# Kernel tuning notes

Measured on AMD Instinct MI355X. Metric: run time of the kernel, lower is better.

The kernel has to match this reference:

```python
import jax, jax.numpy as jnp
import numpy as np

B, N, DEG = 128, 512, 8          # graphs, nodes per graph, avg degree
E = B * N * DEG                  # 524288 edges
F_IN, H1, H2, C = 128, 64, 128, 10
RATIO = 0.8
K = int(np.ceil(RATIO * N))      # TopKPooling keeps ceil(0.8*N)=410 nodes per graph


def setup_inputs() -> dict:
    key = jax.random.key(0)
    ks = jax.random.split(key, 10)
    n_nodes = B * N
    x = jax.random.normal(ks[0], (n_nodes, F_IN), dtype=jnp.float32)
    # random intra-graph edges, then offset node ids per graph
    src = jax.random.randint(ks[1], (B, N * DEG), 0, N)
    dst = jax.random.randint(ks[2], (B, N * DEG), 0, N)
    off = (jnp.arange(B) * N)[:, None]
    edge_index = jnp.stack([(src + off).reshape(-1), (dst + off).reshape(-1)]).astype(jnp.int64)
    batch = jnp.repeat(jnp.arange(B), N).astype(jnp.int64)
    s1 = 1.0 / np.sqrt(F_IN)
    s2 = 1.0 / np.sqrt(H1)
    s3 = 1.0 / np.sqrt(H2)
    return {
        "x": x,
        "edge_index": edge_index,
        "batch": batch,
        "W1": jax.random.uniform(ks[3], (F_IN, H1), jnp.float32, -s1, s1),
        "b1": jnp.zeros((H1,), jnp.float32),
        "W2": jax.random.uniform(ks[4], (H1, H2), jnp.float32, -s2, s2),
        "b2": jnp.zeros((H2,), jnp.float32),
        "pool_w": jax.random.uniform(ks[5], (H2,), jnp.float32, -s3, s3),
        "fc_W": jax.random.uniform(ks[6], (H2, C), jnp.float32, -s3, s3),
        "fc_b": jax.random.uniform(ks[7], (C,), jnp.float32, -s3, s3),
    }


def gcn_conv(x, W, b, src, dst, num_nodes):
    # PyG GCNConv: add self-loops, symmetric normalization, scatter-add aggregation
    loop = jnp.arange(num_nodes)
    src = jnp.concatenate([src, loop])
    dst = jnp.concatenate([dst, loop])
    deg = jax.ops.segment_sum(jnp.ones_like(src, dtype=x.dtype), dst, num_segments=num_nodes)
    dis = jnp.where(deg > 0, jax.lax.rsqrt(jnp.maximum(deg, 1.0)), 0.0)
    norm = dis[src] * dis[dst]                       # [E+N]
    h = x @ W                                        # transform first (smaller of the two in conv1)
    out = jax.ops.segment_sum(norm[:, None] * h[src], dst, num_segments=num_nodes)
    return out + b


def reference(x, edge_index, batch, W1, b1, W2, b2, pool_w, fc_W, fc_b):
    num_nodes = x.shape[0]
    src, dst = edge_index[0], edge_index[1]
    x = jax.nn.relu(gcn_conv(x, W1, b1, src, dst, num_nodes))
    x = jax.nn.relu(gcn_conv(x, W2, b2, src, dst, num_nodes))
    # TopKPooling: score = (x . w)/||w||, per-graph top-k on raw score, gate by tanh(score)
    score = (x @ pool_w) / jnp.linalg.norm(pool_w)   # [B*N]
    score_b = score.reshape(B, N)
    top_vals, top_idx = jax.lax.top_k(score_b, K)    # [B, K]
    x_b = x.reshape(B, N, H2)
    x_sel = jnp.take_along_axis(x_b, top_idx[:, :, None], axis=1)   # [B, K, H2]
    x_sel = x_sel * jnp.tanh(top_vals)[:, :, None]
    # global max pool over each (pooled) graph; pooled edge_index is unused downstream
    g = jnp.max(x_sel, axis=1)                        # [B, H2]
    logits = g @ fc_W + fc_b                          # [B, C]
    return jax.nn.log_softmax(logits, axis=1)
```

## Files before the change

### kernel.cpp

```cpp
#include <hip/hip_runtime.h>
#include <hip/hip_bf16.h>


#define BB 128
#define NN 512
#define NODES (BB*NN)
#define EE (BB*NN*8)
#define EDGPG (NN*8)
#define F_IN 128
#define H1 64
#define H2 128
#define NC 10
#define KSEL 410
#define ROWCAP 48

typedef unsigned short u16;
typedef unsigned int   u32;

static __device__ __forceinline__ float lo2f(u32 u){ return __uint_as_float(u << 16); }
static __device__ __forceinline__ float hi2f(u32 u){ return __uint_as_float(u & 0xffff0000u); }
static __device__ __forceinline__ u16 f2b(float f){
    __hip_bfloat16 h = __float2bfloat16(f);
    return *reinterpret_cast<u16*>(&h);
}
static __device__ __forceinline__ u32 packbf(float a, float b){
    return (u32)f2b(a) | ((u32)f2b(b) << 16);
}
static __device__ __forceinline__ void acc8s(float* a, uint4 v, float ds){
    a[0] = fmaf(ds, lo2f(v.x), a[0]); a[1] = fmaf(ds, hi2f(v.x), a[1]);
    a[2] = fmaf(ds, lo2f(v.y), a[2]); a[3] = fmaf(ds, hi2f(v.y), a[3]);
    a[4] = fmaf(ds, lo2f(v.z), a[4]); a[5] = fmaf(ds, hi2f(v.z), a[5]);
    a[6] = fmaf(ds, lo2f(v.w), a[6]); a[7] = fmaf(ds, hi2f(v.w), a[7]);
}
static __device__ __forceinline__ void acc8(float* a, uint4 v){
    a[0] += lo2f(v.x); a[1] += hi2f(v.x);
    a[2] += lo2f(v.y); a[3] += hi2f(v.y);
    a[4] += lo2f(v.z); a[5] += hi2f(v.z);
    a[6] += lo2f(v.w); a[7] += hi2f(v.w);
}
static __device__ __forceinline__ int swz2048(int bid){
    return ((bid & 7) << 8) | (bid >> 3);
}

static __device__ __forceinline__ bool ei_is_i64(const int* __restrict__ ei){
    return ((ei[1] | ei[3] | ei[5] | ei[7]) == 0);
}
static __device__ __forceinline__ int ld_src(const int* __restrict__ ei, int e, bool w64){
    return w64 ? ei[2*e] : ei[e];
}
static __device__ __forceinline__ int ld_dst(const int* __restrict__ ei, int e, bool w64){
    return w64 ? ei[2*(EE + e)] : ei[EE + e];
}

#define G1NODES 64
#define XPAD 68
__global__ __launch_bounds__(512) void k_prep_gemm1(const int* __restrict__ ei,
                                                    const float* __restrict__ x,
                                                    const float* __restrict__ W1,
                                                    int* __restrict__ cnt,
                                                    int* __restrict__ adj,
                                                    u32* __restrict__ h1u){
    __shared__ __align__(16) float Ws[64*H1];
    __shared__ __align__(16) float xs[G1NODES*XPAD];
    bool w64 = ei_is_i64(ei);
    int t = threadIdx.x;
    int gb = (int)blockIdx.x;
    int b  = gb >> 3;
    int sub = gb & 7;
    int node0 = b*NN + sub*G1NODES;

    int e = b*EDGPG + sub*512 + t;
    int dv = (ld_dst(ei, e, w64) - b*NN) & (NN - 1);
    int sv = ld_src(ei, e, w64) & (NODES - 1);
    int anode = b*NN + dv;
    int p = ROWCAP;

    int tc = t & 15, tr = t >> 4;
    int j0 = tc*4, n0 = tr*2;
    float acc[2][4] = {};

    {
        const float4* Wv0 = (const float4*)W1;
        for (int i = t; i < 1024; i += 512)
            *(float4*)&Ws[i*4] = Wv0[i];
        for (int i = t; i < 1024; i += 512){
            int node = i >> 4, c = i & 15;
            *(float4*)&xs[node*XPAD + c*4] =
                *(const float4*)(x + (size_t)(node0 + node)*F_IN + c*4);
        }
    }
    __syncthreads();
    p = atomicAdd(&cnt[anode], 1);
    const float4* Wv1 = (const float4*)(W1 + 4096);
    float4 wr0 = Wv1[t], wr1 = Wv1[t + 512];
    float4 xr0 = *(const float4*)(x + (size_t)(node0 + (t >> 4))*F_IN + 64 + (t & 15)*4);
    float4 xr1 = *(const float4*)(x + (size_t)(node0 + ((t+512) >> 4))*F_IN + 64 + ((t+512) & 15)*4);

    #pragma unroll 2
    for (int k = 0; k < 64; k += 4){
        float4 xv0 = *(const float4*)&xs[(n0+0)*XPAD + k];
        float4 xv1 = *(const float4*)&xs[(n0+1)*XPAD + k];
        float xa0[4] = {xv0.x, xv0.y, xv0.z, xv0.w};
        float xa1[4] = {xv1.x, xv1.y, xv1.z, xv1.w};
        #pragma unroll
        for (int kk = 0; kk < 4; ++kk){
            float4 wv = *(const float4*)&Ws[(k+kk)*H1 + j0];
            acc[0][0] += xa0[kk]*wv.x; acc[0][1] += xa0[kk]*wv.y; acc[0][2] += xa0[kk]*wv.z; acc[0][3] += xa0[kk]*wv.w;
            acc[1][0] += xa1[kk]*wv.x; acc[1][1] += xa1[kk]*wv.y; acc[1][2] += xa1[kk]*wv.z; acc[1][3] += xa1[kk]*wv.w;
        }
    }
    __syncthreads();
    *(float4*)&Ws[(t      )*4] = wr0;
    *(float4*)&Ws[(t + 512)*4] = wr1;
    *(float4*)&xs[((t      ) >> 4)*XPAD + ((t      ) & 15)*4] = xr0;
    *(float4*)&xs[((t + 512) >> 4)*XPAD + ((t + 512) & 15)*4] = xr1;
    __syncthreads();
    #pragma unroll 2
    for (int k = 0; k < 64; k += 4){
        float4 xv0 = *(const float4*)&xs[(n0+0)*XPAD + k];
        float4 xv1 = *(const float4*)&xs[(n0+1)*XPAD + k];
        float xa0[4] = {xv0.x, xv0.y, xv0.z, xv0.w};
        float xa1[4] = {xv1.x, xv1.y, xv1.z, xv1.w};
        #pragma unroll
        for (int kk = 0; kk < 4; ++kk){
            float4 wv = *(const float4*)&Ws[(k+kk)*H1 + j0];
            acc[0][0] += xa0[kk]*wv.x; acc[0][1] += xa0[kk]*wv.y; acc[0][2] += xa0[kk]*wv.z; acc[0][3] += xa0[kk]*wv.w;
            acc[1][0] += xa1[kk]*wv.x; acc[1][1] += xa1[kk]*wv.y; acc[1][2] += xa1[kk]*wv.z; acc[1][3] += xa1[kk]*wv.w;
        }
    }
    if (p < ROWCAP - 1) adj[anode*ROWCAP + 1 + p] = sv;
    if (t < G1NODES){
        int node = node0 + t;
        adj[node*ROWCAP] = node;
    }
    #pragma unroll
    for (int i = 0; i < 2; ++i){
        int node = node0 + n0 + i;
        size_t base = (size_t)node*32 + tc*2;
        h1u[base]     = packbf(acc[i][0], acc[i][1]);
        h1u[base + 1] = packbf(acc[i][2], acc[i][3]);
    }
}

__global__ __launch_bounds__(256) void k_agg1(const uint4* __restrict__ h1v,
                                              const int* __restrict__ cnt,
                                              const int* __restrict__ adj,
                                              const float4* __restrict__ b1v,
                                              uint4* __restrict__ a1v){
    __shared__ float disl[NN];
    int t = threadIdx.x;
    int lb = swz2048((int)blockIdx.x);
    int node0 = lb*32;
    int node = node0 + (t >> 3);
    int fl = t & 7;
    int rs = node*ROWCAP;
    int cp = cnt[node];
    int4 ap0 = *(const int4*)&adj[rs];
    int4 ap1 = *(const int4*)&adj[rs + 4];
    uint4 vself = h1v[(size_t)node*8 + fl];
    int gbase = node0 & ~(NN - 1);
    for (int i = t; i < NN; i += 256){
        int c = cnt[gbase + i]; if (c > ROWCAP-1) c = ROWCAP-1;
        disl[i] = rsqrtf((float)(c + 1));
    }
    __syncthreads();
    int c = cp; if (c > ROWCAP-1) c = ROWCAP-1;
    int pe = rs + c + 1;
    float a0[8] = {}, a1r[8] = {}, a2r[8] = {}, a3r[8] = {};
    int p = rs;
    if (p + 4 <= pe){
        int s1 = ap0.y, s2 = ap0.z, s3 = ap0.w;
        float d0 = disl[node & (NN-1)];
        float d1 = disl[s1 & (NN-1)], d2 = disl[s2 & (NN-1)], d3 = disl[s3 & (NN-1)];
        uint4 v1 = h1v[s1*8 + fl];
        uint4 v2 = h1v[s2*8 + fl];
        uint4 v3 = h1v[s3*8 + fl];
        acc8s(a0, vself, d0); acc8s(a1r, v1, d1); acc8s(a2r, v2, d2); acc8s(a3r, v3, d3);
        p += 4;
    }
    if (p + 4 <= pe){
        int s0 = ap1.x, s1 = ap1.y, s2 = ap1.z, s3 = ap1.w;
        float d0 = disl[s0 & (NN-1)], d1 = disl[s1 & (NN-1)];
        float d2 = disl[s2 & (NN-1)], d3 = disl[s3 & (NN-1)];
        uint4 v0 = h1v[s0*8 + fl];
        uint4 v1 = h1v[s1*8 + fl];
        uint4 v2 = h1v[s2*8 + fl];
        uint4 v3 = h1v[s3*8 + fl];
        acc8s(a0, v0, d0); acc8s(a1r, v1, d1); acc8s(a2r, v2, d2); acc8s(a3r, v3, d3);
        p += 4;
    }
    for (; p + 4 <= pe; p += 4){
        int s0 = adj[p], s1 = adj[p+1], s2 = adj[p+2], s3 = adj[p+3];
        float d0 = disl[s0 & (NN-1)], d1 = disl[s1 & (NN-1)];
        float d2 = disl[s2 & (NN-1)], d3 = disl[s3 & (NN-1)];
        uint4 v0 = h1v[s0*8 + fl];
        uint4 v1 = h1v[s1*8 + fl];
        uint4 v2 = h1v[s2*8 + fl];
        uint4 v3 = h1v[s3*8 + fl];
        acc8s(a0, v0, d0); acc8s(a1r, v1, d1); acc8s(a2r, v2, d2); acc8s(a3r, v3, d3);
    }
    for (; p < pe; ++p){
        int s = adj[p];
        acc8s(a0, h1v[s*8 + fl], disl[s & (NN-1)]);
    }
    float r[8];
    #pragma unroll
    for (int j = 0; j < 8; ++j) r[j] = (a0[j] + a1r[j]) + (a2r[j] + a3r[j]);
    float dn = disl[node & (NN-1)];
    float4 bA = b1v[2*fl], bB = b1v[2*fl+1];
    float w0 = dn*r[0] + bA.x; w0 = w0 > 0.f ? w0 : 0.f;
    float w1 = dn*r[1] + bA.y; w1 = w1 > 0.f ? w1 : 0.f;
    float w2 = dn*r[2] + bA.z; w2 = w2 > 0.f ? w2 : 0.f;
    float w3 = dn*r[3] + bA.w; w3 = w3 > 0.f ? w3 : 0.f;
    float w4 = dn*r[4] + bB.x; w4 = w4 > 0.f ? w4 : 0.f;
    float w5 = dn*r[5] + bB.y; w5 = w5 > 0.f ? w5 : 0.f;
    float w6 = dn*r[6] + bB.z; w6 = w6 > 0.f ? w6 : 0.f;
    float w7 = dn*r[7] + bB.w; w7 = w7 > 0.f ? w7 : 0.f;
    a1v[node*8 + fl] = make_uint4(packbf(dn*w0, dn*w1), packbf(dn*w2, dn*w3),
                                  packbf(dn*w4, dn*w5), packbf(dn*w6, dn*w7));
}

#define G2NODES 32
#define APAD 68
__global__ __launch_bounds__(256) void k_gemm2s(const uint4* __restrict__ a1v,
                                                const int* __restrict__ cnt,
                                                const int* __restrict__ adj,
                                                const float* __restrict__ W2,
                                                const float* __restrict__ b2,
                                                const float* __restrict__ pw,
                                                u32* __restrict__ a2u,
                                                float* __restrict__ score){
    __shared__ __align__(16) float Ws[32*H2];
    __shared__ __align__(16) float as[G2NODES*APAD];
    __shared__ float pws[H2];
    int t = threadIdx.x;
    int lb = swz2048((int)blockIdx.x);
    int node0 = lb*G2NODES;
    int fl = t & 7, nl = t >> 3;
    int nodeg = node0 + nl;
    int rsg = nodeg*ROWCAP;
    int cp = cnt[nodeg];
    int4 ap0 = *(const int4*)&adj[rsg];
    int4 ap1 = *(const int4*)&adj[rsg + 4];
    uint4 vself = a1v[(size_t)nodeg*8 + fl];
    const float4* Wv0 = (const float4*)W2;
    float4 w0a = Wv0[t], w0b = Wv0[t+256], w0c = Wv0[t+512], w0d = Wv0[t+768];
    if (t < H2) pws[t] = pw[t];
    {
        int c = cp; if (c > ROWCAP-1) c = ROWCAP-1;
        int pe = rsg + c + 1;
        float a0[8] = {}, a1r[8] = {}, a2r[8] = {}, a3r[8] = {};
        int p = rsg;
        if (p + 4 <= pe){
            int s1 = ap0.y, s2 = ap0.z, s3 = ap0.w;
            uint4 v1 = a1v[s1*8 + fl];
            uint4 v2 = a1v[s2*8 + fl];
            uint4 v3 = a1v[s3*8 + fl];
            acc8(a0, vself); acc8(a1r, v1); acc8(a2r, v2); acc8(a3r, v3);
            p += 4;
        }
        if (p + 4 <= pe){
            int s0 = ap1.x, s1 = ap1.y, s2 = ap1.z, s3 = ap1.w;
            uint4 v0 = a1v[s0*8 + fl];
            uint4 v1 = a1v[s1*8 + fl];
            uint4 v2 = a1v[s2*8 + fl];
            uint4 v3 = a1v[s3*8 + fl];
            acc8(a0, v0); acc8(a1r, v1); acc8(a2r, v2); acc8(a3r, v3);
            p += 4;
        }
        for (; p + 4 <= pe; p += 4){
            int s0 = adj[p], s1 = adj[p+1], s2 = adj[p+2], s3 = adj[p+3];
            uint4 v0 = a1v[s0*8 + fl];
            uint4 v1 = a1v[s1*8 + fl];
            uint4 v2 = a1v[s2*8 + fl];
            uint4 v3 = a1v[s3*8 + fl];
            acc8(a0, v0); acc8(a1r, v1); acc8(a2r, v2); acc8(a3r, v3);
        }
        for (; p < pe; ++p){
            uint4 v = a1v[adj[p]*8 + fl];
            acc8(a0, v);
        }
        float dn = rsqrtf((float)(c + 1));
        float* dst = &as[nl*APAD + 8*fl];
        float r0 = dn*((a0[0] + a1r[0]) + (a2r[0] + a3r[0]));
        float r1 = dn*((a0[1] + a1r[1]) + (a2r[1] + a3r[1]));
        float r2 = dn*((a0[2] + a1r[2]) + (a2r[2] + a3r[2]));
        float r3 = dn*((a0[3] + a1r[3]) + (a2r[3] + a3r[3]));
        float r4 = dn*((a0[4] + a1r[4]) + (a2r[4] + a3r[4]));
        float r5 = dn*((a0[5] + a1r[5]) + (a2r[5] + a3r[5]));
        float r6 = dn*((a0[6] + a1r[6]) + (a2r[6] + a3r[6]));
        float r7 = dn*((a0[7] + a1r[7]) + (a2r[7] + a3r[7]));
        *(float4*)&dst[0] = make_float4(r0, r1, r2, r3);
        *(float4*)&dst[4] = make_float4(r4, r5, r6, r7);
    }
    *(float4*)&Ws[(t      )*4] = w0a;
    *(float4*)&Ws[(t + 256)*4] = w0b;
    *(float4*)&Ws[(t + 512)*4] = w0c;
    *(float4*)&Ws[(t + 768)*4] = w0d;
    __syncthreads();
    const float4* Wv1 = (const float4*)(W2 + 4096);
    float4 w1a = Wv1[t], w1b = Wv1[t+256], w1c = Wv1[t+512], w1d = Wv1[t+768];

    int tc = t & 31, tr = t >> 5;
    int j0 = tc*4, n0 = tr*4;
    float acc[4][4] = {};
    #pragma unroll
    for (int half = 0; half < 2; ++half){
        int kb = half*32;
        #pragma unroll 2
        for (int k = 0; k < 32; k += 4){
            float4 xv0 = *(const float4*)&as[(n0+0)*APAD + kb + k];
            float4 xv1 = *(const float4*)&as[(n0+1)*APAD + kb + k];
            float4 xv2 = *(const float4*)&as[(n0+2)*APAD + kb + k];
            float4 xv3 = *(const float4*)&as[(n0+3)*APAD + kb + k];
            float xa0[4] = {xv0.x, xv0.y, xv0.z, xv0.w};
            float xa1[4] = {xv1.x, xv1.y, xv1.z, xv1.w};
            float xa2[4] = {xv2.x, xv2.y, xv2.z, xv2.w};
            float xa3[4] = {xv3.x, xv3.y, xv3.z, xv3.w};
            #pragma unroll
            for (int kk = 0; kk < 4; ++kk){
                float4 wv = *(const float4*)&Ws[(k+kk)*H2 + j0];
                acc[0][0] += xa0[kk]*wv.x; acc[0][1] += xa0[kk]*wv.y; acc[0][2] += xa0[kk]*wv.z; acc[0][3] += xa0[kk]*wv.w;
                acc[1][0] += xa1[kk]*wv.x; acc[1][1] += xa1[kk]*wv.y; acc[1][2] += xa1[kk]*wv.z; acc[1][3] += xa1[kk]*wv.w;
                acc[2][0] += xa2[kk]*wv.x; acc[2][1] += xa2[kk]*wv.y; acc[2][2] += xa2[kk]*wv.z; acc[2][3] += xa2[kk]*wv.w;
                acc[3][0] += xa3[kk]*wv.x; acc[3][1] += xa3[kk]*wv.y; acc[3][2] += xa3[kk]*wv.z; acc[3][3] += xa3[kk]*wv.w;
            }
        }
        if (half == 0){
            __syncthreads();
            *(float4*)&Ws[(t      )*4] = w1a;
            *(float4*)&Ws[(t + 256)*4] = w1b;
            *(float4*)&Ws[(t + 512)*4] = w1c;
            *(float4*)&Ws[(t + 768)*4] = w1d;
            __syncthreads();
        }
    }
    float p0 = pws[j0], p1 = pws[j0+1], p2 = pws[j0+2], p3 = pws[j0+3];
    float bj0 = b2[j0], bj1 = b2[j0+1], bj2 = b2[j0+2], bj3 = b2[j0+3];
    #pragma unroll
    for (int i = 0; i < 4; ++i){
        float v0 = acc[i][0] + bj0; v0 = v0 > 0.f ? v0 : 0.f;
        float v1 = acc[i][1] + bj1; v1 = v1 > 0.f ? v1 : 0.f;
        float v2 = acc[i][2] + bj2; v2 = v2 > 0.f ? v2 : 0.f;
        float v3 = acc[i][3] + bj3; v3 = v3 > 0.f ? v3 : 0.f;
        size_t base = (size_t)(node0 + n0 + i)*64 + tc*2;
        a2u[base]     = packbf(v0, v1);
        a2u[base + 1] = packbf(v2, v3);
        float sp = v0*p0 + v1*p1 + v2*p2 + v3*p3;
        sp += __shfl_xor(sp, 16, 32);
        sp += __shfl_xor(sp,  8, 32);
        sp += __shfl_xor(sp,  4, 32);
        sp += __shfl_xor(sp,  2, 32);
        sp += __shfl_xor(sp,  1, 32);
        if (tc == 0) score[node0 + n0 + i] = sp;
    }
}

__global__ __launch_bounds__(512) void k_pool(const u32* __restrict__ a2u,
                                              const float* __restrict__ score,
                                              const float* __restrict__ pw,
                                              const float* __restrict__ fcW,
                                              const float* __restrict__ fcb,
                                              float* __restrict__ out){
    __shared__ float so[NN];
    __shared__ float ss[NN];
    __shared__ float th[NN];
    __shared__ float pm[32*H2];
    __shared__ float gl[H2];
    __shared__ float fws[H2*NC];
    __shared__ float lg[NC];
    __shared__ float red[3];
    int bid = blockIdx.x, t = threadIdx.x;
    int b = ((bid & 7) << 4) | (bid >> 3);
    float sc = score[b*NN + t];
    for (int i = t; i < H2*NC; i += 512) fws[i] = fcW[i];
    if (t < H2){ float v2 = pw[t]; gl[t] = v2*v2; }
    __syncthreads();
    if (t == 0){
        float s = 0.f;
        for (int i = 0; i < H2; ++i) s += gl[i];
        red[2] = rsqrtf(s);
    }
    __syncthreads();
    float pwinv = red[2];
    so[t] = sc; th[t] = tanhf(sc*pwinv);
    float v = sc;
    for (int k = 2; k <= NN; k <<= 1){
        for (int j = k >> 1; j > 0; j >>= 1){
            bool desc  = ((t & k) == 0);
            bool lower = ((t & j) == 0);
            bool wantmax = (desc == lower);
            float c;
            if (j >= 64){
                ss[t] = v; __syncthreads();
                c = ss[t ^ j];
                __syncthreads();
            } else {
                c = __shfl_xor(v, j, 64);
            }
            v = wantmax ? fmaxf(v, c) : fminf(v, c);
        }
    }
    ss[t] = v;
    __syncthreads();
    float thresh = ss[KSEL-1];
    float mask_t = (so[t] >= thresh) ? 0.f : -INFINITY;
    __syncthreads();
    so[t] = mask_t;
    __syncthreads();
    int tc = t & 15, q = t >> 4;
    const uint4* ap = (const uint4*)(a2u + (size_t)b*NN*64);
    float m0 = -INFINITY, m1 = -INFINITY, m2 = -INFINITY, m3 = -INFINITY;
    float m4 = -INFINITY, m5 = -INFINITY, m6 = -INFINITY, m7 = -INFINITY;
    int nb = q*16;
    #pragma unroll 4
    for (int n = nb; n < nb + 16; ++n){
        uint4 vv = ap[(size_t)n*16 + tc];
        float thn = th[n], son = so[n];
        m0 = fmaxf(m0, lo2f(vv.x)*thn + son);
        m1 = fmaxf(m1, hi2f(vv.x)*thn + son);
        m2 = fmaxf(m2, lo2f(vv.y)*thn + son);
        m3 = fmaxf(m3, hi2f(vv.y)*thn + son);
        m4 = fmaxf(m4, lo2f(vv.z)*thn + son);
        m5 = fmaxf(m5, hi2f(vv.z)*thn + son);
        m6 = fmaxf(m6, lo2f(vv.w)*thn + son);
        m7 = fmaxf(m7, hi2f(vv.w)*thn + son);
    }
    float* pmr = &pm[q*H2 + 8*tc];
    pmr[0] = m0; pmr[1] = m1; pmr[2] = m2; pmr[3] = m3;
    pmr[4] = m4; pmr[5] = m5; pmr[6] = m6; pmr[7] = m7;
    __syncthreads();
    if (t < H2){
        float g = pm[t];
        #pragma unroll
        for (int qq = 1; qq < 32; ++qq) g = fmaxf(g, pm[qq*H2 + t]);
        gl[t] = g;
    }
    __syncthreads();
    if (t < NC){
        float acc = fcb[t];
        for (int k2 = 0; k2 < H2; ++k2) acc += gl[k2]*fws[k2*NC + t];
        lg[t] = acc;
    }
    __syncthreads();
    if (t == 0){
        float mx = lg[0];
        for (int i = 1; i < NC; ++i) mx = fmaxf(mx, lg[i]);
        float s = 0.f;
        for (int i = 0; i < NC; ++i) s += expf(lg[i] - mx);
        red[0] = mx; red[1] = logf(s);
    }
    __syncthreads();
    if (t < NC) out[b*NC + t] = lg[t] - red[0] - red[1];
}

extern "C" void kernel_launch(void* const* d_in, const int* in_sizes, int n_in,
                              void* d_out, int out_size, void* d_ws, size_t ws_size,
                              hipStream_t stream) {
    const float* x   = (const float*)d_in[0];
    const int*   ei  = (const int*)d_in[1];
    const float* W1  = (const float*)d_in[3];
    const float* b1  = (const float*)d_in[4];
    const float* W2  = (const float*)d_in[5];
    const float* b2  = (const float*)d_in[6];
    const float* pw  = (const float*)d_in[7];
    const float* fcW = (const float*)d_in[8];
    const float* fcb = (const float*)d_in[9];

    char* ws = (char*)d_ws;
    int*   cnt   = (int*)(ws + 4096);
    float* score = (float*)(ws + 524288);
    int*   adj   = (int*)(ws + 4194304);
    u32*   h1u   = (u32*)(ws + 16777216);
    u32*   a1u   = (u32*)(ws + 25165824);
    u32*   a2u   = (u32*)(ws + 33554432);

    hipMemsetAsync(cnt, 0, NODES*sizeof(int), stream);
    k_prep_gemm1<<<NODES/G1NODES, 512, 0, stream>>>(ei, x, W1, cnt, adj, h1u);
    k_agg1<<<NODES/32, 256, 0, stream>>>((const uint4*)h1u, cnt, adj,
                                         (const float4*)b1, (uint4*)a1u);
    k_gemm2s<<<NODES/G2NODES, 256, 0, stream>>>((const uint4*)a1u, cnt, adj,
                                                W2, b2, pw, a2u, score);
    k_pool<<<BB, 512, 0, stream>>>(a2u, score, pw, fcW, fcb, (float*)d_out);
}
```

Baseline: 163.3 us.

## Store adjacency as 16-bit local indices and unroll first 16 neighbors

```diff
diff --git a/kernel.cpp b/kernel.cpp
--- a/kernel.cpp
+++ b/kernel.cpp
@@ -41,6 +41,9 @@
 static __device__ __forceinline__ int swz2048(int bid){
     return ((bid & 7) << 8) | (bid >> 3);
 }
+static __device__ __forceinline__ int swz1024(int bid){
+    return ((bid & 7) << 7) | (bid >> 3);
+}
 
 static __device__ __forceinline__ bool ei_is_i64(const int* __restrict__ ei){
     return ((ei[1] | ei[3] | ei[5] | ei[7]) == 0);
@@ -58,20 +61,20 @@
                                                     const float* __restrict__ x,
                                                     const float* __restrict__ W1,
                                                     int* __restrict__ cnt,
-                                                    int* __restrict__ adj,
+                                                    u16* __restrict__ adj,
                                                     u32* __restrict__ h1u){
     __shared__ __align__(16) float Ws[64*H1];
     __shared__ __align__(16) float xs[G1NODES*XPAD];
     bool w64 = ei_is_i64(ei);
     int t = threadIdx.x;
-    int gb = (int)blockIdx.x;
+    int gb = swz1024((int)blockIdx.x);
     int b  = gb >> 3;
     int sub = gb & 7;
     int node0 = b*NN + sub*G1NODES;
 
     int e = b*EDGPG + sub*512 + t;
     int dv = (ld_dst(ei, e, w64) - b*NN) & (NN - 1);
-    int sv = ld_src(ei, e, w64) & (NODES - 1);
+    int sv = ld_src(ei, e, w64) & (NN - 1);
     int anode = b*NN + dv;
     int p = ROWCAP;
 
@@ -128,10 +131,10 @@
             acc[1][0] += xa1[kk]*wv.x; acc[1][1] += xa1[kk]*wv.y; acc[1][2] += xa1[kk]*wv.z; acc[1][3] += xa1[kk]*wv.w;
         }
     }
-    if (p < ROWCAP - 1) adj[anode*ROWCAP + 1 + p] = sv;
+    if (p < ROWCAP - 1) adj[(size_t)anode*ROWCAP + 1 + p] = (u16)sv;
     if (t < G1NODES){
         int node = node0 + t;
-        adj[node*ROWCAP] = node;
+        adj[(size_t)node*ROWCAP] = (u16)(node & (NN - 1));
     }
     #pragma unroll
     for (int i = 0; i < 2; ++i){
@@ -144,69 +147,91 @@
 
 __global__ __launch_bounds__(256) void k_agg1(const uint4* __restrict__ h1v,
                                               const int* __restrict__ cnt,
-                                              const int* __restrict__ adj,
+                                              const u16* __restrict__ adj,
                                               const float4* __restrict__ b1v,
                                               uint4* __restrict__ a1v){
     __shared__ float disl[NN];
     int t = threadIdx.x;
     int lb = swz2048((int)blockIdx.x);
     int node0 = lb*32;
+    int gbase = node0 & ~(NN - 1);
     int node = node0 + (t >> 3);
+    int nl = node & (NN - 1);
     int fl = t & 7;
-    int rs = node*ROWCAP;
+    size_t rs = (size_t)node*ROWCAP;
     int cp = cnt[node];
-    int4 ap0 = *(const int4*)&adj[rs];
-    int4 ap1 = *(const int4*)&adj[rs + 4];
+    uint4 apA = *(const uint4*)&adj[rs];
+    uint4 apB = *(const uint4*)&adj[rs + 8];
     uint4 vself = h1v[(size_t)node*8 + fl];
-    int gbase = node0 & ~(NN - 1);
     for (int i = t; i < NN; i += 256){
         int c = cnt[gbase + i]; if (c > ROWCAP-1) c = ROWCAP-1;
         disl[i] = rsqrtf((float)(c + 1));
     }
     __syncthreads();
     int c = cp; if (c > ROWCAP-1) c = ROWCAP-1;
-    int pe = rs + c + 1;
+    int ne = c + 1;
+    int e1 = (int)(apA.x >> 16);
+    int e2 = (int)(apA.y & 0xffff), e3 = (int)(apA.y >> 16);
+    int e4 = (int)(apA.z & 0xffff), e5 = (int)(apA.z >> 16);
+    int e6 = (int)(apA.w & 0xffff), e7 = (int)(apA.w >> 16);
+    int e8  = (int)(apB.x & 0xffff), e9  = (int)(apB.x >> 16);
+    int e10 = (int)(apB.y & 0xffff), e11 = (int)(apB.y >> 16);
+    int e12 = (int)(apB.z & 0xffff), e13 = (int)(apB.z >> 16);
+    int e14 = (int)(apB.w & 0xffff), e15 = (int)(apB.w >> 16);
     float a0[8] = {}, a1r[8] = {}, a2r[8] = {}, a3r[8] = {};
-    int p = rs;
-    if (p + 4 <= pe){
-        int s1 = ap0.y, s2 = ap0.z, s3 = ap0.w;
-        float d0 = disl[node & (NN-1)];
-        float d1 = disl[s1 & (NN-1)], d2 = disl[s2 & (NN-1)], d3 = disl[s3 & (NN-1)];
-        uint4 v1 = h1v[s1*8 + fl];
-        uint4 v2 = h1v[s2*8 + fl];
-        uint4 v3 = h1v[s3*8 + fl];
+    int p = 0;
+    if (p + 4 <= ne){
+        float d0 = disl[nl], d1 = disl[e1], d2 = disl[e2], d3 = disl[e3];
+        uint4 v1 = h1v[(size_t)(gbase + e1)*8 + fl];
+        uint4 v2 = h1v[(size_t)(gbase + e2)*8 + fl];
+        uint4 v3 = h1v[(size_t)(gbase + e3)*8 + fl];
         acc8s(a0, vself, d0); acc8s(a1r, v1, d1); acc8s(a2r, v2, d2); acc8s(a3r, v3, d3);
         p += 4;
     }
-    if (p + 4 <= pe){
-        int s0 = ap1.x, s1 = ap1.y, s2 = ap1.z, s3 = ap1.w;
-        float d0 = disl[s0 & (NN-1)], d1 = disl[s1 & (NN-1)];
-        float d2 = disl[s2 & (NN-1)], d3 = disl[s3 & (NN-1)];
-        uint4 v0 = h1v[s0*8 + fl];
-        uint4 v1 = h1v[s1*8 + fl];
-        uint4 v2 = h1v[s2*8 + fl];
-        uint4 v3 = h1v[s3*8 + fl];
+    if (p + 4 <= ne){
+        float d0 = disl[e4], d1 = disl[e5], d2 = disl[e6], d3 = disl[e7];
+        uint4 v0 = h1v[(size_t)(gbase + e4)*8 + fl];
+        uint4 v1 = h1v[(size_t)(gbase + e5)*8 + fl];
+        uint4 v2 = h1v[(size_t)(gbase + e6)*8 + fl];
+        uint4 v3 = h1v[(size_t)(gbase + e7)*8 + fl];
         acc8s(a0, v0, d0); acc8s(a1r, v1, d1); acc8s(a2r, v2, d2); acc8s(a3r, v3, d3);
         p += 4;
     }
-    for (; p + 4 <= pe; p += 4){
-        int s0 = adj[p], s1 = adj[p+1], s2 = adj[p+2], s3 = adj[p+3];
-        float d0 = disl[s0 & (NN-1)], d1 = disl[s1 & (NN-1)];
-        float d2 = disl[s2 & (NN-1)], d3 = disl[s3 & (NN-1)];
-        uint4 v0 = h1v[s0*8 + fl];
-        uint4 v1 = h1v[s1*8 + fl];
-        uint4 v2 = h1v[s2*8 + fl];
-        uint4 v3 = h1v[s3*8 + fl];
+    if (p + 4 <= ne){
+        float d0 = disl[e8], d1 = disl[e9], d2 = disl[e10], d3 = disl[e11];
+        uint4 v0 = h1v[(size_t)(gbase + e8 )*8 + fl];
+        uint4 v1 = h1v[(size_t)(gbase + e9 )*8 + fl];
+        uint4 v2 = h1v[(size_t)(gbase + e10)*8 + fl];
+        uint4 v3 = h1v[(size_t)(gbase + e11)*8 + fl];
         acc8s(a0, v0, d0); acc8s(a1r, v1, d1); acc8s(a2r, v2, d2); acc8s(a3r, v3, d3);
-    }
-    for (; p < pe; ++p){
-        int s = adj[p];
-        acc8s(a0, h1v[s*8 + fl], disl[s & (NN-1)]);
+        p += 4;
+    }
+    if (p + 4 <= ne){
+        float d0 = disl[e12], d1 = disl[e13], d2 = disl[e14], d3 = disl[e15];
+        uint4 v0 = h1v[(size_t)(gbase + e12)*8 + fl];
+        uint4 v1 = h1v[(size_t)(gbase + e13)*8 + fl];
+        uint4 v2 = h1v[(size_t)(gbase + e14)*8 + fl];
+        uint4 v3 = h1v[(size_t)(gbase + e15)*8 + fl];
+        acc8s(a0, v0, d0); acc8s(a1r, v1, d1); acc8s(a2r, v2, d2); acc8s(a3r, v3, d3);
+        p += 4;
+    }
+    for (; p + 4 <= ne; p += 4){
+        int s0 = adj[rs+p], s1 = adj[rs+p+1], s2 = adj[rs+p+2], s3 = adj[rs+p+3];
+        float d0 = disl[s0], d1 = disl[s1], d2 = disl[s2], d3 = disl[s3];
+        uint4 v0 = h1v[(size_t)(gbase + s0)*8 + fl];
+        uint4 v1 = h1v[(size_t)(gbase + s1)*8 + fl];
+        uint4 v2 = h1v[(size_t)(gbase + s2)*8 + fl];
+        uint4 v3 = h1v[(size_t)(gbase + s3)*8 + fl];
+        acc8s(a0, v0, d0); acc8s(a1r, v1, d1); acc8s(a2r, v2, d2); acc8s(a3r, v3, d3);
+    }
+    for (; p < ne; ++p){
+        int s = adj[rs + p];
+        acc8s(a0, h1v[(size_t)(gbase + s)*8 + fl], disl[s]);
     }
     float r[8];
     #pragma unroll
     for (int j = 0; j < 8; ++j) r[j] = (a0[j] + a1r[j]) + (a2r[j] + a3r[j]);
-    float dn = disl[node & (NN-1)];
+    float dn = disl[nl];
     float4 bA = b1v[2*fl], bB = b1v[2*fl+1];
     float w0 = dn*r[0] + bA.x; w0 = w0 > 0.f ? w0 : 0.f;
     float w1 = dn*r[1] + bA.y; w1 = w1 > 0.f ? w1 : 0.f;
@@ -224,7 +249,7 @@
 #define APAD 68
 __global__ __launch_bounds__(256) void k_gemm2s(const uint4* __restrict__ a1v,
                                                 const int* __restrict__ cnt,
-                                                const int* __restrict__ adj,
+                                                const u16* __restrict__ adj,
                                                 const float* __restrict__ W2,
                                                 const float* __restrict__ b2,
                                                 const float* __restrict__ pw,
@@ -236,49 +261,72 @@
     int t = threadIdx.x;
     int lb = swz2048((int)blockIdx.x);
     int node0 = lb*G2NODES;
+    int gbase = node0 & ~(NN - 1);
     int fl = t & 7, nl = t >> 3;
     int nodeg = node0 + nl;
-    int rsg = nodeg*ROWCAP;
+    size_t rsg = (size_t)nodeg*ROWCAP;
     int cp = cnt[nodeg];
-    int4 ap0 = *(const int4*)&adj[rsg];
-    int4 ap1 = *(const int4*)&adj[rsg + 4];
+    uint4 apA = *(const uint4*)&adj[rsg];
+    uint4 apB = *(const uint4*)&adj[rsg + 8];
     uint4 vself = a1v[(size_t)nodeg*8 + fl];
     const float4* Wv0 = (const float4*)W2;
     float4 w0a = Wv0[t], w0b = Wv0[t+256], w0c = Wv0[t+512], w0d = Wv0[t+768];
     if (t < H2) pws[t] = pw[t];
     {
         int c = cp; if (c > ROWCAP-1) c = ROWCAP-1;
-        int pe = rsg + c + 1;
+        int ne = c + 1;
+        int e1 = (int)(apA.x >> 16);
+        int e2 = (int)(apA.y & 0xffff), e3 = (int)(apA.y >> 16);
+        int e4 = (int)(apA.z & 0xffff), e5 = (int)(apA.z >> 16);
+        int e6 = (int)(apA.w & 0xffff), e7 = (int)(apA.w >> 16);
+        int e8  = (int)(apB.x & 0xffff), e9  = (int)(apB.x >> 16);
+        int e10 = (int)(apB.y & 0xffff), e11 = (int)(apB.y >> 16);
+        int e12 = (int)(apB.z & 0xffff), e13 = (int)(apB.z >> 16);
+        int e14 = (int)(apB.w & 0xffff), e15 = (int)(apB.w >> 16);
         float a0[8] = {}, a1r[8] = {}, a2r[8] = {}, a3r[8] = {};
-        int p = rsg;
-        if (p + 4 <= pe){
-            int s1 = ap0.y, s2 = ap0.z, s3 = ap0.w;
-            uint4 v1 = a1v[s1*8 + fl];
-            uint4 v2 = a1v[s2*8 + fl];
-            uint4 v3 = a1v[s3*8 + fl];
+        int p = 0;
+        if (p + 4 <= ne){
+            uint4 v1 = a1v[(size_t)(gbase + e1)*8 + fl];
+            uint4 v2 = a1v[(size_t)(gbase + e2)*8 + fl];
+            uint4 v3 = a1v[(size_t)(gbase + e3)*8 + fl];
             acc8(a0, vself); acc8(a1r, v1); acc8(a2r, v2); acc8(a3r, v3);
             p += 4;
         }
-        if (p + 4 <= pe){
-            int s0 = ap1.x, s1 = ap1.y, s2 = ap1.z, s3 = ap1.w;
-            uint4 v0 = a1v[s0*8 + fl];
-            uint4 v1 = a1v[s1*8 + fl];
-            uint4 v2 = a1v[s2*8 + fl];
-            uint4 v3 = a1v[s3*8 + fl];
+        if (p + 4 <= ne){
+            uint4 v0 = a1v[(size_t)(gbase + e4)*8 + fl];
+            uint4 v1 = a1v[(size_t)(gbase + e5)*8 + fl];
+            uint4 v2 = a1v[(size_t)(gbase + e6)*8 + fl];
+            uint4 v3 = a1v[(size_t)(gbase + e7)*8 + fl];
             acc8(a0, v0); acc8(a1r, v1); acc8(a2r, v2); acc8(a3r, v3);
             p += 4;
         }
-        for (; p + 4 <= pe; p += 4){
-            int s0 = adj[p], s1 = adj[p+1], s2 = adj[p+2], s3 = adj[p+3];
-            uint4 v0 = a1v[s0*8 + fl];
-            uint4 v1 = a1v[s1*8 + fl];
-            uint4 v2 = a1v[s2*8 + fl];
-            uint4 v3 = a1v[s3*8 + fl];
+        if (p + 4 <= ne){
+            uint4 v0 = a1v[(size_t)(gbase + e8 )*8 + fl];
+            uint4 v1 = a1v[(size_t)(gbase + e9 )*8 + fl];
+            uint4 v2 = a1v[(size_t)(gbase + e10)*8 + fl];
+            uint4 v3 = a1v[(size_t)(gbase + e11)*8 + fl];
             acc8(a0, v0); acc8(a1r, v1); acc8(a2r, v2); acc8(a3r, v3);
-        }
-        for (; p < pe; ++p){
-            uint4 v = a1v[adj[p]*8 + fl];
-            acc8(a0, v);
+            p += 4;
+        }
+        if (p + 4 <= ne){
+            uint4 v0 = a1v[(size_t)(gbase + e12)*8 + fl];
+            uint4 v1 = a1v[(size_t)(gbase + e13)*8 + fl];
+            uint4 v2 = a1v[(size_t)(gbase + e14)*8 + fl];
+            uint4 v3 = a1v[(size_t)(gbase + e15)*8 + fl];
+            acc8(a0, v0); acc8(a1r, v1); acc8(a2r, v2); acc8(a3r, v3);
+            p += 4;
+        }
+        for (; p + 4 <= ne; p += 4){
+            int s0 = adj[rsg+p], s1 = adj[rsg+p+1], s2 = adj[rsg+p+2], s3 = adj[rsg+p+3];
+            uint4 v0 = a1v[(size_t)(gbase + s0)*8 + fl];
+            uint4 v1 = a1v[(size_t)(gbase + s1)*8 + fl];
+            uint4 v2 = a1v[(size_t)(gbase + s2)*8 + fl];
+            uint4 v3 = a1v[(size_t)(gbase + s3)*8 + fl];
+            acc8(a0, v0); acc8(a1r, v1); acc8(a2r, v2); acc8(a3r, v3);
+        }
+        for (; p < ne; ++p){
+            int s = adj[rsg + p];
+            acc8(a0, a1v[(size_t)(gbase + s)*8 + fl]);
         }
         float dn = rsqrtf((float)(c + 1));
         float* dst = &as[nl*APAD + 8*fl];
@@ -470,7 +518,7 @@
     char* ws = (char*)d_ws;
     int*   cnt   = (int*)(ws + 4096);
     float* score = (float*)(ws + 524288);
-    int*   adj   = (int*)(ws + 4194304);
+    u16*   adj   = (u16*)(ws + 4194304);
     u32*   h1u   = (u32*)(ws + 16777216);
     u32*   a1u   = (u32*)(ws + 25165824);
     u32*   a2u   = (u32*)(ws + 33554432);
```

Result: slower. 182.7 us (+11.9%).
